# Kernel optimization log

Hardware: AMD Instinct MI355X
Metric: run time of the kernel (lower is better)

Reference implementation:

```python
import jax, jax.numpy as jnp
import numpy as np

B, D_K, D_V = 1024, 64, 64
N_FEAT, RANK, K = 32768, 1, 32

def _normalize(a):
    return a / jnp.linalg.norm(a, axis=-1, keepdims=True)

def setup_inputs() -> dict:
    key = jax.random.key(0)
    k0, k1, k2, k3, k4 = jax.random.split(key, 5)
    x = jax.random.normal(k0, (B, D_K, D_V), dtype=jnp.float32)
    V_enc = _normalize(jax.random.normal(k1, (N_FEAT, RANK, D_K), dtype=jnp.float32))
    W_enc = _normalize(jax.random.normal(k2, (N_FEAT, RANK, D_V), dtype=jnp.float32))
    V_dec = _normalize(jax.random.normal(k3, (N_FEAT, RANK, D_K), dtype=jnp.float32))
    W_dec = _normalize(jax.random.normal(k4, (N_FEAT, RANK, D_V), dtype=jnp.float32))
    b_enc = jnp.zeros((N_FEAT,), dtype=jnp.float32)
    bias = jnp.zeros((D_K, D_V), dtype=jnp.float32)
    return {"x": x, "V_enc": V_enc, "W_enc": W_enc, "b_enc": b_enc,
            "V_dec": V_dec, "W_dec": W_dec, "bias": bias}

def reference(x, V_enc, W_enc, b_enc, V_dec, W_dec, bias):
    b, d_k, d_v = x.shape
    n_feat = V_enc.shape[0]
    x_flat = x.reshape(b, d_k * d_v)
    # encode: einsum('irk,bkv,irv->bi') == x_flat @ (sum_r v_ir (x) w_ir)^T
    M_enc = jnp.einsum('irk,irv->ikv', V_enc, W_enc).reshape(n_feat, d_k * d_v)
    pre = x_flat @ M_enc.T + b_enc                       # [B, n_feat]
    # topk activation with relu on the kept values, zeros elsewhere
    vals, idx = jax.lax.top_k(pre, K)                    # [B, K]
    vals = jnp.maximum(vals, 0.0)
    coeffs = jnp.zeros_like(pre).at[jnp.arange(b)[:, None], idx].set(vals)
    # decode: einsum('bi,irk,irv->bkv')
    M_dec = jnp.einsum('irk,irv->ikv', V_dec, W_dec).reshape(n_feat, d_k * d_v)
    recon_flat = coeffs @ M_dec + bias.reshape(-1)
    recon = recon_flat.reshape(b, d_k, d_v)
    mse = jnp.mean((recon_flat - x_flat) ** 2)
    # fresh steps_since_active buffer (zeros) + dead_threshold=100 -> no dead
    # features, so aux_loss == 0 exactly; total loss == mse.
    return recon, coeffs, mse
```

## Files before the change

### kernel.cpp

```cpp
#include <hip/hip_runtime.h>
#include <hip/hip_bf16.h>
#include <hip/hip_fp8.h>
#include <stdint.h>

#define NFEAT 32768
#define BATCH 1024
#define DK 64
#define DV 64
#define DD 4096
#define KSEL 32
#define CAND_CAP 512
#define CAND_TARGET 128

using bf16 = __bf16;
using bf16x8 = __attribute__((ext_vector_type(8))) __bf16;
using f32x4 = __attribute__((ext_vector_type(4))) float;
using f32x16 = __attribute__((ext_vector_type(16))) float;
using i32x4 = __attribute__((ext_vector_type(4))) int;
using i32x8 = __attribute__((ext_vector_type(8))) int;

__device__ __forceinline__ void gload_lds16(const void* g, void* l) {
  __builtin_amdgcn_global_load_lds((const __attribute__((address_space(1))) void*)g,
                                   (__attribute__((address_space(3))) void*)l,
                                   16, 0, 0);
}

__device__ inline unsigned mono16(unsigned u) {
  return (u & 0x8000u) ? ((~u) & 0xFFFFu) : (u | 0x8000u);
}

__global__ void k_convert_x(const float* __restrict__ x, unsigned char* __restrict__ xb, int n) {
  int i = (blockIdx.x * blockDim.x + threadIdx.x) * 16;
  if (i >= n) return;
  union { unsigned char b[16]; uint4 u; } o;
#pragma unroll
  for (int j = 0; j < 16; j += 4) {
    float4 v = *reinterpret_cast<const float4*>(x + i + j);
    o.b[j + 0] = __hip_fp8_e4m3(v.x).__x;
    o.b[j + 1] = __hip_fp8_e4m3(v.y).__x;
    o.b[j + 2] = __hip_fp8_e4m3(v.z).__x;
    o.b[j + 3] = __hip_fp8_e4m3(v.w).__x;
  }
  *reinterpret_cast<uint4*>(xb + i) = o.u;
}

__global__ void k_build_menc(const float* __restrict__ Venc, const float* __restrict__ Wenc,
                             unsigned char* __restrict__ Menc) {
  int i = blockIdx.x;
  int t = threadIdx.x;
  int k = t >> 2;
  int vb = (t & 3) << 4;
  float vk = 16.0f * Venc[i * DK + k];
  const float* wrow = Wenc + i * DV + vb;
  union { unsigned char b[16]; uint4 u; } o;
#pragma unroll
  for (int j = 0; j < 16; j += 4) {
    float4 w = *reinterpret_cast<const float4*>(wrow + j);
    o.b[j + 0] = __hip_fp8_e4m3(vk * w.x).__x;
    o.b[j + 1] = __hip_fp8_e4m3(vk * w.y).__x;
    o.b[j + 2] = __hip_fp8_e4m3(vk * w.z).__x;
    o.b[j + 3] = __hip_fp8_e4m3(vk * w.w).__x;
  }
  *reinterpret_cast<uint4*>(Menc + (size_t)i * DD + (t << 4)) = o.u;
}

#define BM 256
#define BN 256
#define BKB 128
#define NT (DD / BKB)
#define ABUF 32768
#define BUFSZ 65536
#define GEMM_LDS (2 * BUFSZ)

__device__ __forceinline__ void stage_chunk(const unsigned char* __restrict__ G, size_t rowbase,
                                            int kb0, int c, int lane, char* dstbase) {
  int b32 = c >> 2, kg = c & 3;
  const unsigned char* src = G + (rowbase + (size_t)(b32 * 32 + (lane & 31))) * DD + kb0 +
                             kg * 32 + ((lane >> 5) << 4);
  gload_lds16(src, dstbase + c * 1024);
}

__device__ __forceinline__ i32x8 frag_ld8(const char* base, int chunk, int lane) {
  const char* p = base + chunk * 1024 + (lane & 31) * 16;
  i32x4 lo = *reinterpret_cast<const i32x4*>(p);
  i32x4 hi = *reinterpret_cast<const i32x4*>(p + 512);
  i32x8 r;
  r[0] = lo[0]; r[1] = lo[1]; r[2] = lo[2]; r[3] = lo[3];
  r[4] = hi[0]; r[5] = hi[1]; r[6] = hi[2]; r[7] = hi[3];
  return r;
}

__device__ __forceinline__ int chA(int half, int idx) {
  int g = idx >> 2, kg = idx & 3;
  int mb32 = (g & 1) + ((g >> 1) << 2) + half * 2;
  return mb32 * 4 + kg;
}
__device__ __forceinline__ int chB(int half, int idx) {
  int nb32 = ((idx >> 2) << 1) + half;
  return nb32 * 4 + (idx & 3);
}

#define LD_A(H)                                                                     \
  _Pragma("unroll") for (int mb = 0; mb < 2; ++mb)                                  \
  _Pragma("unroll") for (int kh = 0; kh < 2; ++kh)                                  \
    afr[mb][kh] = frag_ld8(cur, (wr * 4 + (H) * 2 + mb) * 4 + kh * 2 + (lane >> 5), lane);

#define LD_B(H)                                                                     \
  _Pragma("unroll") for (int kh = 0; kh < 2; ++kh)                                  \
    bfr[(H)][kh] = frag_ld8(cur + ABUF, (wc * 2 + (H)) * 4 + kh * 2 + (lane >> 5), lane);

#define ST_A(HALF, KT)                                                              \
  stage_chunk(A, brow, (KT) * BKB, chA(HALF, wave * 2), lane, nxt);                 \
  stage_chunk(A, brow, (KT) * BKB, chA(HALF, wave * 2 + 1), lane, nxt);

#define ST_B(HALF, KT)                                                              \
  stage_chunk(Bt, bcol, (KT) * BKB, chB(HALF, wave * 2), lane, nxt + ABUF);         \
  stage_chunk(Bt, bcol, (KT) * BKB, chB(HALF, wave * 2 + 1), lane, nxt + ABUF);

#define MFMA_Q(MH, NB)                                                              \
  asm volatile("s_waitcnt lgkmcnt(0)" ::: "memory");                                \
  __builtin_amdgcn_sched_barrier(0);                                                \
  __builtin_amdgcn_s_setprio(1);                                                    \
  _Pragma("unroll") for (int mb = 0; mb < 2; ++mb)                                  \
  _Pragma("unroll") for (int kh = 0; kh < 2; ++kh)                                  \
    acc[(MH) * 2 + mb][NB] = __builtin_amdgcn_mfma_scale_f32_32x32x64_f8f6f4(       \
        afr[mb][kh], bfr[NB][kh], acc[(MH) * 2 + mb][NB], 0, 0, 0, 0x7F, 0, 0x7F);  \
  __builtin_amdgcn_s_setprio(0);

#define VMC(N) asm volatile("s_waitcnt vmcnt(" #N ")" ::: "memory");
#define LGKM0 asm volatile("s_waitcnt lgkmcnt(0)" ::: "memory");
#define BARR                                                                        \
  asm volatile("s_barrier" ::: "memory");                                           \
  __builtin_amdgcn_sched_barrier(0);

__global__ __launch_bounds__(512, 2)
void k_gemm(const unsigned char* __restrict__ A, const unsigned char* __restrict__ Bt,
            const float* __restrict__ benc, bf16* __restrict__ C) {
  extern __shared__ char lds[];
  int tid = threadIdx.x;
  int wave = tid >> 6;
  int lane = tid & 63;
  int wr = wave >> 2;
  int wc = wave & 3;

  int d = blockIdx.x;
  int lw = (d & 7) * 64 + (d >> 3);
  int q = lw >> 2;
  int p = lw & 3;
  size_t brow = (size_t)p * BM;
  size_t bcol = (size_t)q * BN;

  f32x16 acc[4][2] = {};
  i32x8 afr[2][2];
  i32x8 bfr[2][2];

  {
    char* nxt = lds;
    ST_B(0, 0) ST_A(0, 0) ST_B(1, 0) ST_A(1, 0)
  }
  VMC(4)
  BARR

#pragma unroll 1
  for (int u = 0; u < NT - 1; ++u) {
    char* cur = lds + (u & 1) * BUFSZ;
    char* nxt = lds + ((u + 1) & 1) * BUFSZ;
    int k1 = u + 1;
    LD_A(0) LD_B(0)
    ST_B(0, k1)
    VMC(4)
    BARR
    MFMA_Q(0, 0)
    LD_B(1)
    ST_A(0, k1)
    VMC(4)
    BARR
    MFMA_Q(0, 1)
    LD_A(1)
    ST_B(1, k1) ST_A(1, k1)
    VMC(4)
    LGKM0
    BARR
    MFMA_Q(1, 1)
    MFMA_Q(1, 0)
  }

  {
    char* cur = lds + ((NT - 1) & 1) * BUFSZ;
    LD_A(0) LD_B(0)
    VMC(2)
    BARR
    MFMA_Q(0, 0)
    LD_B(1)
    VMC(0)
    BARR
    MFMA_Q(0, 1)
    LD_A(1)
    LGKM0
    BARR
    MFMA_Q(1, 1)
    MFMA_Q(1, 0)
  }

#pragma unroll
  for (int nb = 0; nb < 2; ++nb) {
    size_t col = bcol + wc * 64 + nb * 32 + (lane & 31);
    float be = benc[col];
#pragma unroll
    for (int MB = 0; MB < 4; ++MB) {
      size_t row0 = brow + wr * 128 + MB * 32 + ((lane >> 5) << 2);
#pragma unroll
      for (int reg = 0; reg < 16; ++reg) {
        size_t row = row0 + (reg & 3) + ((reg >> 2) << 3);
        C[row * NFEAT + col] = (bf16)(acc[MB][nb][reg] * 0.0625f + be);
      }
    }
  }
}

__global__ void k_topk(const unsigned short* __restrict__ pre, int* __restrict__ cand_idx,
                       int* __restrict__ cand_cnt, float* __restrict__ coeffs) {
  __shared__ int hist[8192];
  __shared__ int csum[256];
  __shared__ int sBstar;
  __shared__ int scount;
  int b = blockIdx.x;
  int t = threadIdx.x;
  const unsigned short* row = pre + (size_t)b * NFEAT;
  for (int i = t; i < 8192; i += 256) hist[i] = 0;
  if (t == 0) scount = 0;
  __syncthreads();

  for (int i = (t << 3); i < NFEAT; i += 2048) {
    uint4 v = *reinterpret_cast<const uint4*>(row + i);
#pragma unroll
    for (int j = 0; j < 4; ++j) {
      unsigned w = (&v.x)[j];
      atomicAdd(&hist[mono16(w & 0xFFFFu) >> 3], 1);
      atomicAdd(&hist[mono16(w >> 16) >> 3], 1);
    }
  }
  __syncthreads();

  int s = 0;
  for (int i = 0; i < 32; ++i) s += hist[t * 32 + i];
  csum[t] = s;
  __syncthreads();
  int suff = 0;
  for (int j = t + 1; j < 256; ++j) suff += csum[j];
  if (suff < CAND_TARGET && suff + s >= CAND_TARGET) {
    int acc = suff;
    int bstar = t * 32;
    for (int i = 31; i >= 0; --i) {
      acc += hist[t * 32 + i];
      if (acc >= CAND_TARGET) { bstar = t * 32 + i; break; }
    }
    sBstar = bstar;
  }
  __syncthreads();
  int Bstar = sBstar;
  int* cidx = cand_idx + b * CAND_CAP;

  for (int i = (t << 3); i < NFEAT; i += 2048) {
    uint4 v = *reinterpret_cast<const uint4*>(row + i);
#pragma unroll
    for (int j = 0; j < 4; ++j) {
      unsigned w = (&v.x)[j];
      int b0 = (int)(mono16(w & 0xFFFFu) >> 3);
      int b1 = (int)(mono16(w >> 16) >> 3);
      if (b0 >= Bstar) { int p2 = atomicAdd(&scount, 1); if (p2 < CAND_CAP) cidx[p2] = i + j * 2; }
      if (b1 >= Bstar) { int p2 = atomicAdd(&scount, 1); if (p2 < CAND_CAP) cidx[p2] = i + j * 2 + 1; }
    }
  }
  __syncthreads();
  if (t == 0) cand_cnt[b] = (scount < CAND_CAP) ? scount : CAND_CAP;

  float* crow = coeffs + (size_t)b * NFEAT;
  float4 z4 = {0.f, 0.f, 0.f, 0.f};
  for (int i = (t << 2); i < NFEAT; i += 1024)
    *reinterpret_cast<float4*>(crow + i) = z4;
}

__global__ void k_refine(const float* __restrict__ x,
                         const float* __restrict__ Venc,
                         const float* __restrict__ Wenc,
                         const float* __restrict__ benc,
                         const float* __restrict__ Vdec,
                         const float* __restrict__ Wdec,
                         const float* __restrict__ bias,
                         const int* __restrict__ cand_idx,
                         const int* __restrict__ cand_cnt,
                         float* __restrict__ recon,
                         float* __restrict__ coeffs,
                         float* __restrict__ msepart) {
  __shared__ float rval[CAND_CAP];
  __shared__ int ridx[CAND_CAP];
  __shared__ float selv[KSEL];
  __shared__ int seli[KSEL];
  __shared__ float Vd[KSEL][DK];
  __shared__ float Wd[KSEL][DV];
  __shared__ float red[256];

  int b = blockIdx.x;
  int t = threadIdx.x;
  int wave = t >> 6;
  int lane = t & 63;

  const float* xr = x + (size_t)b * DD;

  float xreg[DK];
#pragma unroll
  for (int kk = 0; kk < DK; ++kk)
    xreg[kk] = xr[kk * DV + lane];

  int c = cand_cnt[b];
  if (c > CAND_CAP) c = CAND_CAP;
  for (int i = t; i < c; i += 256) ridx[i] = cand_idx[b * CAND_CAP + i];
  __syncthreads();

  for (int j = wave; j < c; j += 4) {
    int fi = __builtin_amdgcn_readfirstlane(ridx[j]);
    const float* vr = Venc + (size_t)fi * DK;
    float w = Wenc[(size_t)fi * DV + lane];
    float a0 = 0.f, a1 = 0.f, a2 = 0.f, a3 = 0.f;
#pragma unroll
    for (int kk = 0; kk < DK; kk += 4) {
      a0 = fmaf(xreg[kk + 0], vr[kk + 0], a0);
      a1 = fmaf(xreg[kk + 1], vr[kk + 1], a1);
      a2 = fmaf(xreg[kk + 2], vr[kk + 2], a2);
      a3 = fmaf(xreg[kk + 3], vr[kk + 3], a3);
    }
    float p2 = ((a0 + a1) + (a2 + a3)) * w;
#pragma unroll
    for (int off = 1; off < 64; off <<= 1) p2 += __shfl_xor(p2, off);
    if (lane == 0) rval[j] = p2 + benc[fi];
  }
  __syncthreads();

  for (int t2 = t; t2 < c; t2 += 256) {
    float v = rval[t2];
    int fi = ridx[t2];
    int rank = 0;
    for (int j = 0; j < c; ++j) {
      float vj = rval[j];
      if (vj > v || (vj == v && ridx[j] < fi)) ++rank;
    }
    if (rank < KSEL) { selv[rank] = v; seli[rank] = fi; }
  }
  __syncthreads();

  if (t < KSEL) {
    float v = fmaxf(selv[t], 0.f);
    selv[t] = v;
    coeffs[(size_t)b * NFEAT + seli[t]] = v;
  }
  __syncthreads();

  for (int i = t; i < KSEL * DK; i += 256) {
    int s = i >> 6, e = i & 63;
    Vd[s][e] = Vdec[(size_t)seli[s] * DK + e];
    Wd[s][e] = Wdec[(size_t)seli[s] * DV + e];
  }
  __syncthreads();

  int k = t >> 2;
  int vb = (t & 3) << 4;
  float4 r4[4];
#pragma unroll
  for (int g = 0; g < 4; ++g)
    r4[g] = *reinterpret_cast<const float4*>(bias + k * DV + vb + g * 4);
#pragma unroll
  for (int s = 0; s < KSEL; ++s) {
    float a = selv[s] * Vd[s][k];
    const float4* wrow = reinterpret_cast<const float4*>(&Wd[s][vb]);
#pragma unroll
    for (int g = 0; g < 4; ++g) {
      float4 wv = wrow[g];
      r4[g].x = fmaf(a, wv.x, r4[g].x);
      r4[g].y = fmaf(a, wv.y, r4[g].y);
      r4[g].z = fmaf(a, wv.z, r4[g].z);
      r4[g].w = fmaf(a, wv.w, r4[g].w);
    }
  }
  float m = 0.f;
  float* ro = recon + (size_t)b * DD + k * DV + vb;
#pragma unroll
  for (int g = 0; g < 4; ++g) {
    float4 xv = *reinterpret_cast<const float4*>(xr + k * DV + vb + g * 4);
    float dx = r4[g].x - xv.x, dy = r4[g].y - xv.y;
    float dz = r4[g].z - xv.z, dw = r4[g].w - xv.w;
    m = fmaf(dx, dx, m); m = fmaf(dy, dy, m);
    m = fmaf(dz, dz, m); m = fmaf(dw, dw, m);
    *reinterpret_cast<float4*>(ro + g * 4) = r4[g];
  }
  red[t] = m;
  __syncthreads();
  for (int s2 = 128; s2 > 0; s2 >>= 1) {
    if (t < s2) red[t] += red[t + s2];
    __syncthreads();
  }
  if (t == 0) msepart[b] = red[0];
}

__global__ void k_mse(const float* __restrict__ msepart, float* __restrict__ out) {
  __shared__ float red[256];
  int t = threadIdx.x;
  float s = 0.f;
  for (int i = t; i < BATCH; i += 256) s += msepart[i];
  red[t] = s;
  __syncthreads();
  for (int k = 128; k > 0; k >>= 1) {
    if (t < k) red[t] += red[t + k];
    __syncthreads();
  }
  if (t == 0) out[0] = red[0] / (float)((size_t)BATCH * DD);
}

extern "C" void kernel_launch(void* const* d_in, const int* in_sizes, int n_in,
                              void* d_out, int out_size, void* d_ws, size_t ws_size,
                              hipStream_t stream) {
  const float* x    = (const float*)d_in[0];
  const float* Venc = (const float*)d_in[1];
  const float* Wenc = (const float*)d_in[2];
  const float* benc = (const float*)d_in[3];
  const float* Vdec = (const float*)d_in[4];
  const float* Wdec = (const float*)d_in[5];
  const float* bias = (const float*)d_in[6];

  float* out = (float*)d_out;
  float* recon  = out;
  float* coeffs = out + (size_t)BATCH * DD;
  float* mse    = coeffs + (size_t)BATCH * NFEAT;

  char* wsp = (char*)d_ws;
  unsigned char* xb8 = (unsigned char*)wsp;   wsp += (size_t)BATCH * DD;
  unsigned char* Menc8 = (unsigned char*)wsp; wsp += (size_t)NFEAT * DD;
  int* cand_idx = (int*)wsp;                  wsp += (size_t)BATCH * CAND_CAP * sizeof(int);
  int* cand_cnt = (int*)wsp;                  wsp += (size_t)BATCH * sizeof(int);
  float* msepart = (float*)wsp;               wsp += (size_t)BATCH * sizeof(float);
  bf16* pre = (bf16*)wsp;                     wsp += (size_t)BATCH * NFEAT * sizeof(bf16);

  hipFuncSetAttribute((const void*)k_gemm, hipFuncAttributeMaxDynamicSharedMemorySize,
                      GEMM_LDS);

  k_convert_x<<<(BATCH * DD) / (256 * 16), 256, 0, stream>>>(x, xb8, BATCH * DD);
  k_build_menc<<<NFEAT, 256, 0, stream>>>(Venc, Wenc, Menc8);
  k_gemm<<<(BATCH / BM) * (NFEAT / BN), 512, GEMM_LDS, stream>>>(xb8, Menc8, benc, pre);
  k_topk<<<BATCH, 256, 0, stream>>>((const unsigned short*)pre, cand_idx, cand_cnt, coeffs);
  k_refine<<<BATCH, 256, 0, stream>>>(x, Venc, Wenc, benc, Vdec, Wdec, bias,
                                      cand_idx, cand_cnt, recon, coeffs, msepart);
  k_mse<<<1, 256, 0, stream>>>(msepart, mse);
}
```

Baseline: 315.7 us.

## Pre-tile fp8 GEMM operands so each LDS chunk is one contiguous 1KB block

The fp8 conversion kernels for x and M_enc now write their output in a blocked layout, grouping 32 rows by 32-byte k-slices, so each 1 KB staging chunk sits contiguously in global memory. The GEMM staging loads become fully contiguous 16-byte-per-lane reads instead of 32 rows strided by 4096 bytes. This aims to improve global-load coalescing and cache/TLB behaviour in the main GEMM. In exchange, the producer kernels do narrower 4-byte stores, and build_menc runs a 128-iteration loop per block with fewer blocks.

```diff
diff --git a/kernel.cpp b/kernel.cpp
--- a/kernel.cpp
+++ b/kernel.cpp
@@ -13,7 +13,6 @@
 #define CAND_TARGET 128
 
 using bf16 = __bf16;
-using bf16x8 = __attribute__((ext_vector_type(8))) __bf16;
 using f32x4 = __attribute__((ext_vector_type(4))) float;
 using f32x16 = __attribute__((ext_vector_type(16))) float;
 using i32x4 = __attribute__((ext_vector_type(4))) int;
@@ -29,39 +28,47 @@
   return (u & 0x8000u) ? ((~u) & 0xFFFFu) : (u | 0x8000u);
 }
 
-__global__ void k_convert_x(const float* __restrict__ x, unsigned char* __restrict__ xb, int n) {
-  int i = (blockIdx.x * blockDim.x + threadIdx.x) * 16;
-  if (i >= n) return;
-  union { unsigned char b[16]; uint4 u; } o;
-#pragma unroll
-  for (int j = 0; j < 16; j += 4) {
-    float4 v = *reinterpret_cast<const float4*>(x + i + j);
-    o.b[j + 0] = __hip_fp8_e4m3(v.x).__x;
-    o.b[j + 1] = __hip_fp8_e4m3(v.y).__x;
-    o.b[j + 2] = __hip_fp8_e4m3(v.z).__x;
-    o.b[j + 3] = __hip_fp8_e4m3(v.w).__x;
-  }
-  *reinterpret_cast<uint4*>(xb + i) = o.u;
+
+__global__ void k_convert_x(const float* __restrict__ x, unsigned char* __restrict__ xb) {
+  int t = threadIdx.x;
+  int rb = blockIdx.x >> 3;
+  int kg0 = (blockIdx.x & 7) * 16;
+  int row = (t & 127) >> 2;
+  int cin = ((t >> 7) << 4) + ((t & 3) << 2);
+  const float* xrow = x + ((size_t)rb * 32 + row) * DD;
+  for (int kg = kg0; kg < kg0 + 16; ++kg) {
+    float4 v = *reinterpret_cast<const float4*>(xrow + kg * 32 + cin);
+    union { unsigned char b[4]; unsigned u; } o;
+    o.b[0] = __hip_fp8_e4m3(v.x).__x;
+    o.b[1] = __hip_fp8_e4m3(v.y).__x;
+    o.b[2] = __hip_fp8_e4m3(v.z).__x;
+    o.b[3] = __hip_fp8_e4m3(v.w).__x;
+    *reinterpret_cast<unsigned*>(xb + (((size_t)rb * 128 + kg) << 10) + t * 4) = o.u;
+  }
 }
 
 __global__ void k_build_menc(const float* __restrict__ Venc, const float* __restrict__ Wenc,
                              unsigned char* __restrict__ Menc) {
-  int i = blockIdx.x;
   int t = threadIdx.x;
-  int k = t >> 2;
-  int vb = (t & 3) << 4;
-  float vk = 16.0f * Venc[i * DK + k];
-  const float* wrow = Wenc + i * DV + vb;
-  union { unsigned char b[16]; uint4 u; } o;
-#pragma unroll
-  for (int j = 0; j < 16; j += 4) {
-    float4 w = *reinterpret_cast<const float4*>(wrow + j);
-    o.b[j + 0] = __hip_fp8_e4m3(vk * w.x).__x;
-    o.b[j + 1] = __hip_fp8_e4m3(vk * w.y).__x;
-    o.b[j + 2] = __hip_fp8_e4m3(vk * w.z).__x;
-    o.b[j + 3] = __hip_fp8_e4m3(vk * w.w).__x;
-  }
-  *reinterpret_cast<uint4*>(Menc + (size_t)i * DD + (t << 4)) = o.u;
+  int rb = blockIdx.x;
+  int row = (t & 127) >> 2;
+  int cin = ((t >> 7) << 4) + ((t & 3) << 2);
+  size_t rowg = (size_t)rb * 32 + row;
+  const float* vrow = Venc + rowg * DK;
+  float4 w0 = *reinterpret_cast<const float4*>(Wenc + rowg * DV + cin);
+  float4 w1 = *reinterpret_cast<const float4*>(Wenc + rowg * DV + 32 + cin);
+  unsigned char* base = Menc + ((size_t)rb << 17);
+#pragma unroll 4
+  for (int kg = 0; kg < 128; ++kg) {
+    float vk = 16.0f * vrow[kg >> 1];
+    float4 w = (kg & 1) ? w1 : w0;
+    union { unsigned char b[4]; unsigned u; } o;
+    o.b[0] = __hip_fp8_e4m3(vk * w.x).__x;
+    o.b[1] = __hip_fp8_e4m3(vk * w.y).__x;
+    o.b[2] = __hip_fp8_e4m3(vk * w.z).__x;
+    o.b[3] = __hip_fp8_e4m3(vk * w.w).__x;
+    *reinterpret_cast<unsigned*>(base + (kg << 10) + t * 4) = o.u;
+  }
 }
 
 #define BM 256
@@ -72,11 +79,9 @@
 #define BUFSZ 65536
 #define GEMM_LDS (2 * BUFSZ)
 
-__device__ __forceinline__ void stage_chunk(const unsigned char* __restrict__ G, size_t rowbase,
-                                            int kb0, int c, int lane, char* dstbase) {
-  int b32 = c >> 2, kg = c & 3;
-  const unsigned char* src = G + (rowbase + (size_t)(b32 * 32 + (lane & 31))) * DD + kb0 +
-                             kg * 32 + ((lane >> 5) << 4);
+__device__ __forceinline__ void stage_chunk(const unsigned char* __restrict__ G, size_t r32base,
+                                            int kg0, int c, int lane, char* dstbase) {
+  const unsigned char* src = G + (((r32base + (c >> 2)) * 128 + kg0 + (c & 3)) << 10) + lane * 16;
   gload_lds16(src, dstbase + c * 1024);
 }
 
@@ -110,12 +115,12 @@
     bfr[(H)][kh] = frag_ld8(cur + ABUF, (wc * 2 + (H)) * 4 + kh * 2 + (lane >> 5), lane);
 
 #define ST_A(HALF, KT)                                                              \
-  stage_chunk(A, brow, (KT) * BKB, chA(HALF, wave * 2), lane, nxt);                 \
-  stage_chunk(A, brow, (KT) * BKB, chA(HALF, wave * 2 + 1), lane, nxt);
+  stage_chunk(A, ar32, (KT) * 4, chA(HALF, wave * 2), lane, nxt);                   \
+  stage_chunk(A, ar32, (KT) * 4, chA(HALF, wave * 2 + 1), lane, nxt);
 
 #define ST_B(HALF, KT)                                                              \
-  stage_chunk(Bt, bcol, (KT) * BKB, chB(HALF, wave * 2), lane, nxt + ABUF);         \
-  stage_chunk(Bt, bcol, (KT) * BKB, chB(HALF, wave * 2 + 1), lane, nxt + ABUF);
+  stage_chunk(Bt, br32, (KT) * 4, chB(HALF, wave * 2), lane, nxt + ABUF);           \
+  stage_chunk(Bt, br32, (KT) * 4, chB(HALF, wave * 2 + 1), lane, nxt + ABUF);
 
 #define MFMA_Q(MH, NB)                                                              \
   asm volatile("s_waitcnt lgkmcnt(0)" ::: "memory");                                \
@@ -149,6 +154,8 @@
   int p = lw & 3;
   size_t brow = (size_t)p * BM;
   size_t bcol = (size_t)q * BN;
+  size_t ar32 = brow >> 5;
+  size_t br32 = bcol >> 5;
 
   f32x16 acc[4][2] = {};
   i32x8 afr[2][2];
@@ -443,8 +450,8 @@
   hipFuncSetAttribute((const void*)k_gemm, hipFuncAttributeMaxDynamicSharedMemorySize,
                       GEMM_LDS);
 
-  k_convert_x<<<(BATCH * DD) / (256 * 16), 256, 0, stream>>>(x, xb8, BATCH * DD);
-  k_build_menc<<<NFEAT, 256, 0, stream>>>(Venc, Wenc, Menc8);
+  k_convert_x<<<256, 256, 0, stream>>>(x, xb8);
+  k_build_menc<<<NFEAT / 32, 256, 0, stream>>>(Venc, Wenc, Menc8);
   k_gemm<<<(BATCH / BM) * (NFEAT / BN), 512, GEMM_LDS, stream>>>(xb8, Menc8, benc, pre);
   k_topk<<<BATCH, 256, 0, stream>>>((const unsigned short*)pre, cand_idx, cand_cnt, coeffs);
   k_refine<<<BATCH, 256, 0, stream>>>(x, Venc, Wenc, benc, Vdec, Wdec, bias,
```

Result: faster. 296.3 us (-6.1%).
